# Performance work log

Hardware: AMD Instinct MI355X
Metric: run time of the kernel (lower is better)

Reference implementation:

```python
import jax, jax.numpy as jnp
import numpy as np

WIN = 8
HEADS = 4
DHEAD = 32
HID = HEADS * DHEAD  # 128


def setup_inputs() -> dict:
    key = jax.random.key(0)
    k1, k2, k3, k4 = jax.random.split(key, 4)
    x = jax.random.normal(k1, (1, 64, 48, 48, 48), dtype=jnp.float32)
    w_qkv = jax.random.normal(k2, (3 * HID, 64), dtype=jnp.float32) * 0.05  # Conv3d 1x1, no bias
    w_out = jax.random.normal(k3, (64, HID), dtype=jnp.float32) * 0.05     # merge_heads Conv3d 1x1
    b_out = jax.random.normal(k4, (64,), dtype=jnp.float32) * 0.05
    return {"x": x, "w_qkv": w_qkv, "w_out": w_out, "b_out": b_out}


def reference(x, w_qkv, w_out, b_out):
    B, C, H, W, D = x.shape
    X, Y, Z = H // WIN, W // WIN, D // WIN
    # 1x1x1 conv == channel matmul
    qkv = jnp.einsum('bcxyz,oc->boxyz', x, w_qkv)  # [B, 3*h*c, H, W, D]
    t = qkv.reshape(B, 3, HEADS, DHEAD, X, WIN, Y, WIN, Z, WIN)
    # -> [3, B, X, Y, Z, h, wx, wy, wz, c]
    t = t.transpose(1, 0, 4, 6, 8, 2, 5, 7, 9, 3)
    t = t.reshape(3, B * X * Y * Z, HEADS, WIN ** 3, DHEAD)
    q, k, v = t[0], t[1], t[2]
    scale = 1.0 / jnp.sqrt(jnp.asarray(DHEAD, dtype=q.dtype))
    scores = jnp.einsum('whnc,whmc->whnm', q, k) * scale  # [windows, h, 512, 512]
    attn = jax.nn.softmax(scores, axis=-1)
    out = jnp.einsum('whnm,whmc->whnc', attn, v)
    # merge windows back: -> [B, h*c, H, W, D]
    out = out.reshape(B, X, Y, Z, HEADS, WIN, WIN, WIN, DHEAD)
    out = out.transpose(0, 4, 8, 1, 5, 2, 6, 3, 7).reshape(B, HID, H, W, D)
    return jnp.einsum('bcxyz,oc->boxyz', out, w_out) + b_out[None, :, None, None, None]
```

## Files before the change

kernel.cpp:

```cpp
#include <hip/hip_runtime.h>
#include <hip/hip_bf16.h>
#include <stdint.h>

#define NWIN 216
#define NVOX 110592

typedef __bf16 bf16_t;
typedef __attribute__((ext_vector_type(8))) __bf16 bf16x8;
typedef __attribute__((ext_vector_type(4))) __bf16 bf16x4;
typedef __attribute__((ext_vector_type(4))) float f32x4;
typedef __attribute__((ext_vector_type(16))) float f32x16;
typedef __attribute__((ext_vector_type(4))) unsigned int u32x4;
typedef __attribute__((ext_vector_type(2))) unsigned int u32x2;

__device__ __forceinline__ f32x4 mfma16(bf16x8 a, bf16x8 b, f32x4 c) {
  return __builtin_amdgcn_mfma_f32_16x16x32_bf16(a, b, c, 0, 0, 0);
}
__device__ __forceinline__ f32x16 mfma32(bf16x8 a, bf16x8 b, f32x16 c) {
  return __builtin_amdgcn_mfma_f32_32x32x16_bf16(a, b, c, 0, 0, 0);
}

__device__ __forceinline__ float fexp2(float x) {
  return __builtin_amdgcn_exp2f(x);
}

__device__ __forceinline__ unsigned int pk2(float lo, float hi) {
  unsigned short l = __builtin_bit_cast(unsigned short, (bf16_t)lo);
  unsigned short h = __builtin_bit_cast(unsigned short, (bf16_t)hi);
  return (unsigned int)l | ((unsigned int)h << 16);
}

__device__ __forceinline__ void swap_half(unsigned int& a, unsigned int& b) {
#if __has_builtin(__builtin_amdgcn_permlane32_swap)
  u32x2 r = __builtin_amdgcn_permlane32_swap(a, b, false, false);
  a = r[0]; b = r[1];
#else
  asm("v_permlane32_swap_b32 %0, %1" : "+v"(a), "+v"(b));
#endif
}

__global__ __launch_bounds__(512, 1) void qkv_kernel(const float* __restrict__ x,
                                                     const float* __restrict__ w_qkv,
                                                     bf16_t* __restrict__ qkv) {
  __shared__ bf16_t xs[512][72];
  __shared__ bf16_t wsm[384][72];
  const int w = blockIdx.x;
  const int wx = w / 36, wy = (w / 6) % 6, wz = w % 6;
  const int t = threadIdx.x;
  const int lane = t & 63;
  const int q16 = lane & 15, g = lane >> 4;
  const float SC = 0.25505003946337226f;

  #pragma unroll
  for (int i = 0; i < 12; ++i) {
    int seg = t + 512 * i;
    int o = seg >> 4, cq = (seg & 15) << 2;
    float4 v4 = reinterpret_cast<const float4*>(w_qkv)[seg];
    float sc = (o < 128) ? SC : 1.0f;
    bf16_t* dst = &wsm[o][cq];
    dst[0] = (bf16_t)(v4.x * sc); dst[1] = (bf16_t)(v4.y * sc);
    dst[2] = (bf16_t)(v4.z * sc); dst[3] = (bf16_t)(v4.w * sc);
  }
  #pragma unroll
  for (int i = 0; i < 4; ++i) {
    int seg = t + 512 * i;
    int cpair = seg & 31, xy = seg >> 5;
    int ix = xy >> 3, iy = xy & 7;
    const float* s0 = x + (((2 * cpair) * 48 + wx * 8 + ix) * 48 + wy * 8 + iy) * 48 + wz * 8;
    const float* s1 = s0 + 48 * 48 * 48;
    float4 a0 = reinterpret_cast<const float4*>(s0)[0];
    float4 a1 = reinterpret_cast<const float4*>(s0)[1];
    float4 b0 = reinterpret_cast<const float4*>(s1)[0];
    float4 b1 = reinterpret_cast<const float4*>(s1)[1];
    float av[8] = {a0.x, a0.y, a0.z, a0.w, a1.x, a1.y, a1.z, a1.w};
    float bv[8] = {b0.x, b0.y, b0.z, b0.w, b1.x, b1.y, b1.z, b1.w};
    #pragma unroll
    for (int z = 0; z < 8; ++z)
      *(unsigned int*)&xs[xy * 8 + z][2 * cpair] = pk2(av[z], bv[z]);
  }
  __syncthreads();

  const int wv = t >> 6;
  bf16x8 aw[3][2];
  #pragma unroll
  for (int j = 0; j < 3; ++j)
    #pragma unroll
    for (int s = 0; s < 2; ++s)
      aw[j][s] = *(const bf16x8*)&wsm[wv * 48 + j * 16 + q16][s * 32 + 8 * g];

  for (int nt = 0; nt < 32; ++nt) {
    int n = nt * 16 + q16;
    bf16x8 xb0 = *(const bf16x8*)&xs[n][8 * g];
    bf16x8 xb1 = *(const bf16x8*)&xs[n][32 + 8 * g];
    #pragma unroll
    for (int j = 0; j < 3; ++j) {
      f32x4 acc = {0.f, 0.f, 0.f, 0.f};
      acc = mfma16(aw[j][0], xb0, acc);
      acc = mfma16(aw[j][1], xb1, acc);
      int ob = wv * 48 + j * 16 + 4 * g;
      int sel = ob >> 7, rem = ob & 127, hh = rem >> 5, dd = rem & 31;
      bf16x4 pk;
      pk[0] = (bf16_t)acc[0]; pk[1] = (bf16_t)acc[1];
      pk[2] = (bf16_t)acc[2]; pk[3] = (bf16_t)acc[3];
      *(bf16x4*)(qkv + ((((size_t)sel * NWIN + w) * 4 + hh) * 512 + n) * 32 + dd) = pk;
    }
  }
}


__device__ __forceinline__ void attn_step(bf16x8 kf0, bf16x8 kf1, bf16x8 vf0, bf16x8 vf1,
                                          bf16x8 q0, bf16x8 q1, const f32x16& z, bf16x8 ones,
                                          f32x16& O, f32x16& Sm) {
  f32x16 S = mfma32(kf0, q0, z);
  S = mfma32(kf1, q1, S);
  #pragma unroll
  for (int r = 0; r < 16; ++r) S[r] = fexp2(S[r]);
  unsigned int p01 = pk2(S[0], S[1]),   p23 = pk2(S[2], S[3]);
  unsigned int p45 = pk2(S[4], S[5]),   p67 = pk2(S[6], S[7]);
  unsigned int p89 = pk2(S[8], S[9]),   pab = pk2(S[10], S[11]);
  unsigned int pcd = pk2(S[12], S[13]), pef = pk2(S[14], S[15]);
  swap_half(p01, p45);
  swap_half(p23, p67);
  swap_half(p89, pcd);
  swap_half(pab, pef);
  u32x4 u0 = {p01, p23, p45, p67};
  u32x4 u1 = {p89, pab, pcd, pef};
  bf16x8 pf0 = __builtin_bit_cast(bf16x8, u0);
  bf16x8 pf1 = __builtin_bit_cast(bf16x8, u1);
  O = mfma32(pf0, vf0, O);
  O = mfma32(pf1, vf1, O);
  Sm = mfma32(pf0, ones, Sm);
  Sm = mfma32(pf1, ones, Sm);
}

__global__ __launch_bounds__(512, 2) void attn_kernel(const bf16_t* __restrict__ qkv,
                                                      bf16_t* __restrict__ att) {
  __shared__ bf16_t vt[32][520];
  const int blk = blockIdx.x;
  const int w = blk >> 2, h = blk & 3;
  const bf16_t* qb = qkv + ((size_t)(0 * NWIN + w) * 4 + h) * 16384;
  const bf16_t* kb = qkv + ((size_t)(1 * NWIN + w) * 4 + h) * 16384;
  const bf16_t* vb = qkv + ((size_t)(2 * NWIN + w) * 4 + h) * 16384;
  const int t = threadIdx.x, lane = t & 63, wv = t >> 6;
  const int l31 = lane & 31, hi = lane >> 5;

  bf16x8 qf[2][2];
  #pragma unroll
  for (int qs = 0; qs < 2; ++qs)
    #pragma unroll
    for (int c = 0; c < 2; ++c)
      qf[qs][c] = *(const bf16x8*)(qb + (wv * 64 + qs * 32 + l31) * 32 + c * 16 + 8 * hi);

  #pragma unroll
  for (int i = 0; i < 2; ++i) {
    int task = i * 512 + t;
    int p = task >> 2, dg = task & 3;
    bf16x8 v0 = *(const bf16x8*)(vb + (2 * p) * 32 + 8 * dg);
    bf16x8 v1 = *(const bf16x8*)(vb + (2 * p + 1) * 32 + 8 * dg);
    u32x4 a = __builtin_bit_cast(u32x4, v0);
    u32x4 b = __builtin_bit_cast(u32x4, v1);
    #pragma unroll
    for (int j = 0; j < 4; ++j) {
      unsigned int lo = (a[j] & 0xffffu) | (b[j] << 16);
      unsigned int hh = (a[j] >> 16) | (b[j] & 0xffff0000u);
      *(unsigned int*)&vt[dg * 8 + 2 * j][2 * p]     = lo;
      *(unsigned int*)&vt[dg * 8 + 2 * j + 1][2 * p] = hh;
    }
  }
  __syncthreads();

  f32x16 O0 = {}, O1 = {};
  f32x16 Sm0 = {}, Sm1 = {};
  const f32x16 z = {};
  bf16x8 ones;
  #pragma unroll
  for (int e = 0; e < 8; ++e) ones[e] = (bf16_t)1.0f;

  const bf16_t* kptr = kb + l31 * 32 + 8 * hi;
  bf16x8 kf0 = *(const bf16x8*)(kptr);
  bf16x8 kf1 = *(const bf16x8*)(kptr + 16);
  for (int kt = 0; kt < 15; ++kt) {
    const bf16_t* nk = kptr + (kt + 1) * 1024;
    bf16x8 nkf0 = *(const bf16x8*)(nk);
    bf16x8 nkf1 = *(const bf16x8*)(nk + 16);
    bf16x8 vf0 = *(const bf16x8*)&vt[l31][kt * 32 + 8 * hi];
    bf16x8 vf1 = *(const bf16x8*)&vt[l31][kt * 32 + 8 * hi + 16];
    attn_step(kf0, kf1, vf0, vf1, qf[0][0], qf[0][1], z, ones, O0, Sm0);
    attn_step(kf0, kf1, vf0, vf1, qf[1][0], qf[1][1], z, ones, O1, Sm1);
    kf0 = nkf0; kf1 = nkf1;
  }
  {
    bf16x8 vf0 = *(const bf16x8*)&vt[l31][15 * 32 + 8 * hi];
    bf16x8 vf1 = *(const bf16x8*)&vt[l31][15 * 32 + 8 * hi + 16];
    attn_step(kf0, kf1, vf0, vf1, qf[0][0], qf[0][1], z, ones, O0, Sm0);
    attn_step(kf0, kf1, vf0, vf1, qf[1][0], qf[1][1], z, ones, O1, Sm1);
  }

  #pragma unroll
  for (int qs = 0; qs < 2; ++qs) {
    const f32x16& O = qs ? O1 : O0;
    const f32x16& Sm = qs ? Sm1 : Sm0;
    #pragma unroll
    for (int r = 0; r < 16; ++r) {
      int qr = (r & 3) + 8 * (r >> 2) + 4 * hi;
      int n = wv * 64 + qs * 32 + qr;
      float ri = __builtin_amdgcn_rcpf(Sm[r]);
      att[((size_t)w * 512 + n) * 128 + h * 32 + l31] = (bf16_t)(O[r] * ri);
    }
  }
}

__global__ __launch_bounds__(256) void proj_kernel(const bf16_t* __restrict__ att,
                                                   const float* __restrict__ w_out,
                                                   const float* __restrict__ b_out,
                                                   float* __restrict__ out) {
  const int blk = blockIdx.x;
  const int w = blk >> 1, half = blk & 1;
  const int wx = w / 36, wy = (w / 6) % 6, wz = w % 6;
  const int t = threadIdx.x, lane = t & 63, wv = t >> 6;
  const int q16 = lane & 15, g = lane >> 4;

  bf16x8 aw[4][4];
  #pragma unroll
  for (int ot = 0; ot < 4; ++ot)
    #pragma unroll
    for (int kc = 0; kc < 4; ++kc) {
      const float* wr = w_out + (ot * 16 + q16) * 128 + kc * 32 + 8 * g;
      float4 u0 = reinterpret_cast<const float4*>(wr)[0];
      float4 u1 = reinterpret_cast<const float4*>(wr)[1];
      bf16x8 f;
      f[0]=(bf16_t)u0.x; f[1]=(bf16_t)u0.y; f[2]=(bf16_t)u0.z; f[3]=(bf16_t)u0.w;
      f[4]=(bf16_t)u1.x; f[5]=(bf16_t)u1.y; f[6]=(bf16_t)u1.z; f[7]=(bf16_t)u1.w;
      aw[ot][kc] = f;
    }
  float4 bias[4];
  #pragma unroll
  for (int ot = 0; ot < 4; ++ot)
    bias[ot] = *reinterpret_cast<const float4*>(b_out + ot * 16 + 4 * g);

  #pragma unroll
  for (int i = 0; i < 4; ++i) {
    int n = half * 256 + (wv * 4 + i) * 16 + q16;
    const bf16_t* ar = att + ((size_t)w * 512 + n) * 128;
    bf16x8 bf[4];
    #pragma unroll
    for (int kc = 0; kc < 4; ++kc)
      bf[kc] = *(const bf16x8*)(ar + kc * 32 + 8 * g);
    int ix = n >> 6, iy = (n >> 3) & 7, iz = n & 7;
    int v = ((wx * 8 + ix) * 48 + wy * 8 + iy) * 48 + wz * 8 + iz;
    #pragma unroll
    for (int ot = 0; ot < 4; ++ot) {
      f32x4 acc = {0.f, 0.f, 0.f, 0.f};
      #pragma unroll
      for (int kc = 0; kc < 4; ++kc)
        acc = mfma16(aw[ot][kc], bf[kc], acc);
      #pragma unroll
      for (int r = 0; r < 4; ++r) {
        int o = ot * 16 + 4 * g + r;
        out[(size_t)o * NVOX + v] = acc[r] + ((const float*)&bias[ot])[r];
      }
    }
  }
}

extern "C" void kernel_launch(void* const* d_in, const int* in_sizes, int n_in,
                              void* d_out, int out_size, void* d_ws, size_t ws_size,
                              hipStream_t stream) {
  const float* x     = (const float*)d_in[0];
  const float* w_qkv = (const float*)d_in[1];
  const float* w_out = (const float*)d_in[2];
  const float* b_out = (const float*)d_in[3];
  float* out = (float*)d_out;
  bf16_t* qkv = (bf16_t*)d_ws;
  bf16_t* att = (bf16_t*)((char*)d_ws + (size_t)3 * NWIN * 4 * 512 * 32 * 2);
  qkv_kernel<<<dim3(NWIN), dim3(512), 0, stream>>>(x, w_qkv, qkv);
  attn_kernel<<<dim3(NWIN * 4), dim3(512), 0, stream>>>(qkv, att);
  proj_kernel<<<dim3(NWIN * 2), dim3(256), 0, stream>>>(att, w_out, b_out, out);
}
```

Before: 111.1 us.

## Split attention blocks over query halves and load qkv weights directly to registers

```diff
diff --git a/kernel.cpp b/kernel.cpp
--- a/kernel.cpp
+++ b/kernel.cpp
@@ -39,11 +39,10 @@
 #endif
 }
 
-__global__ __launch_bounds__(512, 1) void qkv_kernel(const float* __restrict__ x,
+__global__ __launch_bounds__(512, 2) void qkv_kernel(const float* __restrict__ x,
                                                      const float* __restrict__ w_qkv,
                                                      bf16_t* __restrict__ qkv) {
   __shared__ bf16_t xs[512][72];
-  __shared__ bf16_t wsm[384][72];
   const int w = blockIdx.x;
   const int wx = w / 36, wy = (w / 6) % 6, wz = w % 6;
   const int t = threadIdx.x;
@@ -51,16 +50,6 @@
   const int q16 = lane & 15, g = lane >> 4;
   const float SC = 0.25505003946337226f;
 
-  #pragma unroll
-  for (int i = 0; i < 12; ++i) {
-    int seg = t + 512 * i;
-    int o = seg >> 4, cq = (seg & 15) << 2;
-    float4 v4 = reinterpret_cast<const float4*>(w_qkv)[seg];
-    float sc = (o < 128) ? SC : 1.0f;
-    bf16_t* dst = &wsm[o][cq];
-    dst[0] = (bf16_t)(v4.x * sc); dst[1] = (bf16_t)(v4.y * sc);
-    dst[2] = (bf16_t)(v4.z * sc); dst[3] = (bf16_t)(v4.w * sc);
-  }
   #pragma unroll
   for (int i = 0; i < 4; ++i) {
     int seg = t + 512 * i;
@@ -78,15 +67,25 @@
     for (int z = 0; z < 8; ++z)
       *(unsigned int*)&xs[xy * 8 + z][2 * cpair] = pk2(av[z], bv[z]);
   }
-  __syncthreads();
 
   const int wv = t >> 6;
   bf16x8 aw[3][2];
   #pragma unroll
-  for (int j = 0; j < 3; ++j)
-    #pragma unroll
-    for (int s = 0; s < 2; ++s)
-      aw[j][s] = *(const bf16x8*)&wsm[wv * 48 + j * 16 + q16][s * 32 + 8 * g];
+  for (int j = 0; j < 3; ++j) {
+    int o = wv * 48 + j * 16 + q16;
+    float sc = (o < 128) ? SC : 1.0f;
+    #pragma unroll
+    for (int s = 0; s < 2; ++s) {
+      const float* wr = w_qkv + o * 64 + s * 32 + 8 * g;
+      float4 u0 = reinterpret_cast<const float4*>(wr)[0];
+      float4 u1 = reinterpret_cast<const float4*>(wr)[1];
+      bf16x8 f;
+      f[0]=(bf16_t)(u0.x*sc); f[1]=(bf16_t)(u0.y*sc); f[2]=(bf16_t)(u0.z*sc); f[3]=(bf16_t)(u0.w*sc);
+      f[4]=(bf16_t)(u1.x*sc); f[5]=(bf16_t)(u1.y*sc); f[6]=(bf16_t)(u1.z*sc); f[7]=(bf16_t)(u1.w*sc);
+      aw[j][s] = f;
+    }
+  }
+  __syncthreads();
 
   for (int nt = 0; nt < 32; ++nt) {
     int n = nt * 16 + q16;
@@ -137,19 +136,17 @@
                                                       bf16_t* __restrict__ att) {
   __shared__ bf16_t vt[32][520];
   const int blk = blockIdx.x;
-  const int w = blk >> 2, h = blk & 3;
+  const int wh = blk >> 1, half = blk & 1;
+  const int w = wh >> 2, h = wh & 3;
   const bf16_t* qb = qkv + ((size_t)(0 * NWIN + w) * 4 + h) * 16384;
   const bf16_t* kb = qkv + ((size_t)(1 * NWIN + w) * 4 + h) * 16384;
   const bf16_t* vb = qkv + ((size_t)(2 * NWIN + w) * 4 + h) * 16384;
   const int t = threadIdx.x, lane = t & 63, wv = t >> 6;
   const int l31 = lane & 31, hi = lane >> 5;
-
-  bf16x8 qf[2][2];
-  #pragma unroll
-  for (int qs = 0; qs < 2; ++qs)
-    #pragma unroll
-    for (int c = 0; c < 2; ++c)
-      qf[qs][c] = *(const bf16x8*)(qb + (wv * 64 + qs * 32 + l31) * 32 + c * 16 + 8 * hi);
+  const int qbase = half * 256 + wv * 32;
+
+  bf16x8 qf0 = *(const bf16x8*)(qb + (qbase + l31) * 32 + 8 * hi);
+  bf16x8 qf1 = *(const bf16x8*)(qb + (qbase + l31) * 32 + 16 + 8 * hi);
 
   #pragma unroll
   for (int i = 0; i < 2; ++i) {
@@ -169,8 +166,7 @@
   }
   __syncthreads();
 
-  f32x16 O0 = {}, O1 = {};
-  f32x16 Sm0 = {}, Sm1 = {};
+  f32x16 O = {}, Sm = {};
   const f32x16 z = {};
   bf16x8 ones;
   #pragma unroll
@@ -185,28 +181,21 @@
     bf16x8 nkf1 = *(const bf16x8*)(nk + 16);
     bf16x8 vf0 = *(const bf16x8*)&vt[l31][kt * 32 + 8 * hi];
     bf16x8 vf1 = *(const bf16x8*)&vt[l31][kt * 32 + 8 * hi + 16];
-    attn_step(kf0, kf1, vf0, vf1, qf[0][0], qf[0][1], z, ones, O0, Sm0);
-    attn_step(kf0, kf1, vf0, vf1, qf[1][0], qf[1][1], z, ones, O1, Sm1);
+    attn_step(kf0, kf1, vf0, vf1, qf0, qf1, z, ones, O, Sm);
     kf0 = nkf0; kf1 = nkf1;
   }
   {
     bf16x8 vf0 = *(const bf16x8*)&vt[l31][15 * 32 + 8 * hi];
     bf16x8 vf1 = *(const bf16x8*)&vt[l31][15 * 32 + 8 * hi + 16];
-    attn_step(kf0, kf1, vf0, vf1, qf[0][0], qf[0][1], z, ones, O0, Sm0);
-    attn_step(kf0, kf1, vf0, vf1, qf[1][0], qf[1][1], z, ones, O1, Sm1);
-  }
-
-  #pragma unroll
-  for (int qs = 0; qs < 2; ++qs) {
-    const f32x16& O = qs ? O1 : O0;
-    const f32x16& Sm = qs ? Sm1 : Sm0;
-    #pragma unroll
-    for (int r = 0; r < 16; ++r) {
-      int qr = (r & 3) + 8 * (r >> 2) + 4 * hi;
-      int n = wv * 64 + qs * 32 + qr;
-      float ri = __builtin_amdgcn_rcpf(Sm[r]);
-      att[((size_t)w * 512 + n) * 128 + h * 32 + l31] = (bf16_t)(O[r] * ri);
-    }
+    attn_step(kf0, kf1, vf0, vf1, qf0, qf1, z, ones, O, Sm);
+  }
+
+  #pragma unroll
+  for (int r = 0; r < 16; ++r) {
+    int qr = (r & 3) + 8 * (r >> 2) + 4 * hi;
+    int n = qbase + qr;
+    float ri = __builtin_amdgcn_rcpf(Sm[r]);
+    att[((size_t)w * 512 + n) * 128 + h * 32 + l31] = (bf16_t)(O[r] * ri);
   }
 }
 
@@ -274,6 +263,6 @@
   bf16_t* qkv = (bf16_t*)d_ws;
   bf16_t* att = (bf16_t*)((char*)d_ws + (size_t)3 * NWIN * 4 * 512 * 32 * 2);
   qkv_kernel<<<dim3(NWIN), dim3(512), 0, stream>>>(x, w_qkv, qkv);
-  attn_kernel<<<dim3(NWIN * 4), dim3(512), 0, stream>>>(qkv, att);
+  attn_kernel<<<dim3(NWIN * 4 * 2), dim3(512), 0, stream>>>(qkv, att);
   proj_kernel<<<dim3(NWIN * 2), dim3(256), 0, stream>>>(att, w_out, b_out, out);
 }
```

New measurement: 110.8 us. About the same (-0.3%).
